# Optimization experiments

Hardware: AMD Instinct MI355X
Metric: run time of the kernel (lower is better)

The kernel has to match this reference:

```python
import jax, jax.numpy as jnp
import numpy as np

N = 50000
E = 800000
IN_C, C1, C2 = 256, 128, 64
BN_EPS = 1e-5


def setup_inputs() -> dict:
    key = jax.random.key(0)
    ks = jax.random.split(key, 12)
    x = jax.random.normal(ks[0], (N, IN_C), dtype=jnp.float32)
    edge_index = jax.random.randint(ks[1], (2, E), 0, N, dtype=jnp.int32)
    edge_weight = jax.random.uniform(ks[2], (E,), dtype=jnp.float32)
    W1 = jax.random.normal(ks[3], (IN_C, C1), dtype=jnp.float32) * 0.05
    b1 = jnp.zeros((C1,), dtype=jnp.float32)
    W2 = jax.random.normal(ks[4], (C1, C2), dtype=jnp.float32) * 0.05
    b2 = jnp.zeros((C2,), dtype=jnp.float32)
    g1 = jnp.ones((C1,), dtype=jnp.float32)
    be1 = jnp.zeros((C1,), dtype=jnp.float32)
    g2 = jnp.ones((C2,), dtype=jnp.float32)
    be2 = jnp.zeros((C2,), dtype=jnp.float32)
    Ws = jax.random.normal(ks[5], (IN_C, C2), dtype=jnp.float32) * 0.05
    bs = jnp.zeros((C2,), dtype=jnp.float32)
    return dict(x=x, edge_index=edge_index, edge_weight=edge_weight,
                W1=W1, b1=b1, W2=W2, b2=b2, g1=g1, be1=be1, g2=g2, be2=be2,
                Ws=Ws, bs=bs)


def _gcn_conv(h_in, row, col, ew, W, b):
    # PyG GCNConv: transform then symmetric-normalized aggregation with self-loops
    n = h_in.shape[0]
    h = h_in @ W  # [N, C]
    loop = jnp.arange(n, dtype=row.dtype)
    row_f = jnp.concatenate([row, loop])
    col_f = jnp.concatenate([col, loop])
    ew_f = jnp.concatenate([ew, jnp.ones((n,), dtype=ew.dtype)])
    deg = jax.ops.segment_sum(ew_f, col_f, num_segments=n)  # degree at targets
    dinv = jnp.where(deg > 0, jax.lax.rsqrt(deg), 0.0)
    norm = dinv[row_f] * ew_f * dinv[col_f]  # [E+N]
    out = jax.ops.segment_sum(h[row_f] * norm[:, None], col_f, num_segments=n)
    return out + b


def _batchnorm(x, gamma, beta):
    mu = jnp.mean(x, axis=0)
    var = jnp.mean(jnp.square(x - mu), axis=0)  # biased, as torch BN forward
    return (x - mu) * jax.lax.rsqrt(var + BN_EPS) * gamma + beta


def reference(x, edge_index, edge_weight, W1, b1, W2, b2, g1, be1, g2, be2, Ws, bs):
    row, col = edge_index[0], edge_index[1]
    skip = x @ Ws + bs
    x1 = _gcn_conv(x, row, col, edge_weight, W1, b1)
    x1 = jax.nn.gelu(_batchnorm(x1, g1, be1), approximate=False)
    # dropout is identity in deterministic/eval reference
    x2 = _gcn_conv(x1, row, col, edge_weight, W2, b2)
    x2 = _batchnorm(x2, g2, be2) + skip
    return x2
```

## Files before the change

### kernel.cpp

```cpp
#include <hip/hip_runtime.h>
#include <math.h>

constexpr int NN = 50000;
constexpr int EE = 800000;
constexpr int INC = 256, CC1 = 128, CC2 = 64;
constexpr int CAP = 56;

typedef short bf16x8 __attribute__((ext_vector_type(8)));
typedef float f32x4 __attribute__((ext_vector_type(4)));

__device__ __forceinline__ unsigned short f2bf(float f) {
    unsigned int u = __builtin_bit_cast(unsigned int, f);
    u = (u + 0x7FFFu + ((u >> 16) & 1u)) >> 16;
    return (unsigned short)u;
}
__device__ __forceinline__ float bf2f(unsigned short u) {
    return __builtin_bit_cast(float, (unsigned int)u << 16);
}
__device__ __forceinline__ float bflo(unsigned int w) {
    return __builtin_bit_cast(float, w << 16);
}
__device__ __forceinline__ float bfhi(unsigned int w) {
    return __builtin_bit_cast(float, w & 0xFFFF0000u);
}
__device__ __forceinline__ unsigned int packbf2(float lo, float hi) {
    return (unsigned int)f2bf(lo) | ((unsigned int)f2bf(hi) << 16);
}
__device__ __forceinline__ float dinv_of(unsigned long long pk) {
    return rsqrtf(1.0f + (float)(unsigned int)pk * (1.0f / 16777216.0f));
}

__global__ void zero_kernel(unsigned long long* __restrict__ packed,
                            float* __restrict__ stats) {
    int i = blockIdx.x * 256 + threadIdx.x;
    if (i < NN) packed[i] = 0ULL;
    if (i < 384) stats[i] = 0.0f;
}

__global__ void __launch_bounds__(256) gemm1_rank_kernel(
        const float* __restrict__ A, const float* __restrict__ B1, const float* __restrict__ B2,
        unsigned short* __restrict__ C1, unsigned short* __restrict__ C2,
        const int* __restrict__ row, const int* __restrict__ col, const float* __restrict__ ew,
        unsigned long long* __restrict__ packed, int2* __restrict__ pairs, int gemm_blocks) {
    constexpr int K = INC, N1 = CC1, N2 = CC2, NT = N1 + N2;
    constexpr int KC = K / 8, PITCH = K + 8;
    __shared__ unsigned short Blds[64 * PITCH];

    if ((int)blockIdx.x >= gemm_blocks) {
        int e = (blockIdx.x - gemm_blocks) * 256 + threadIdx.x;
        if (e < EE) {
            int c = col[e], r = row[e];
            float w = ew[e];
            unsigned int fx = __float2uint_rn(w * 16777216.0f);
            unsigned long long old =
                atomicAdd(&packed[c], (1ULL << 32) | (unsigned long long)fx);
            unsigned int rk = (unsigned int)(old >> 32);
            if (rk < CAP)
                pairs[(long long)c * CAP + rk] = make_int2(r, __float_as_int(w));
        }
        return;
    }

    const int tid = threadIdx.x;
    const int wave = tid >> 6, lane = tid & 63;
    const int quad = lane >> 4, nIdx = lane & 15;
    const int row0 = blockIdx.x * 64 + wave * 16;
    const int arow = row0 + nIdx;
    const int arow_c = (arow < NN) ? arow : (NN - 1);

    bf16x8 afrag[K / 32];
    {
        const float* ap = A + (long long)arow_c * K + quad * 8;
#pragma unroll
        for (int s = 0; s < K / 32; s++) {
            float4 lo = *(const float4*)(ap + s * 32);
            float4 hi = *(const float4*)(ap + s * 32 + 4);
            bf16x8 f;
            f[0] = (short)f2bf(lo.x); f[1] = (short)f2bf(lo.y);
            f[2] = (short)f2bf(lo.z); f[3] = (short)f2bf(lo.w);
            f[4] = (short)f2bf(hi.x); f[5] = (short)f2bf(hi.y);
            f[6] = (short)f2bf(hi.z); f[7] = (short)f2bf(hi.w);
            afrag[s] = f;
        }
    }

    for (int g0 = 0; g0 < NT; g0 += 64) {
        if (g0) __syncthreads();
        {
            int n = tid & 63;
            int gcol = g0 + n;
            const float* Bp = B1; int Nw = N1; int bcol = gcol;
            if (gcol >= N1) { Bp = B2; Nw = N2; bcol = gcol - N1; }
            for (int kc = tid >> 6; kc < KC; kc += 4) {
                int k0 = kc * 8;
                bf16x8 v;
#pragma unroll
                for (int j = 0; j < 8; j++)
                    v[j] = (short)f2bf(Bp[(long long)(k0 + j) * Nw + bcol]);
                *(bf16x8*)(&Blds[n * PITCH + k0]) = v;
            }
        }
        __syncthreads();
#pragma unroll
        for (int t4 = 0; t4 < 4; t4++) {
            const unsigned short* bp = &Blds[(t4 * 16 + nIdx) * PITCH + quad * 8];
            f32x4 acc = {0.0f, 0.0f, 0.0f, 0.0f};
#pragma unroll
            for (int s = 0; s < K / 32; s++) {
                bf16x8 bf = *(const bf16x8*)(bp + s * 32);
                acc = __builtin_amdgcn_mfma_f32_16x16x32_bf16(afrag[s], bf, acc, 0, 0, 0);
            }
            int ocol = g0 + t4 * 16 + nIdx;
#pragma unroll
            for (int r = 0; r < 4; r++) {
                int orow = row0 + quad * 4 + r;
                if (orow < NN) {
                    if (ocol < N1)
                        C1[(long long)orow * N1 + ocol] = f2bf(acc[r]);
                    else
                        C2[(long long)orow * N2 + (ocol - N1)] = f2bf(acc[r]);
                }
            }
        }
    }
}

__global__ void __launch_bounds__(256) gather1_kernel(
        const unsigned short* __restrict__ h, const unsigned long long* __restrict__ packed,
        const float* __restrict__ b1, const int2* __restrict__ pairs,
        unsigned short* __restrict__ aggb, float* __restrict__ stats) {
    const int tid = threadIdx.x;
    const int gi = blockIdx.x * 256 + tid;
    const int node = gi >> 4;
    const int part = tid & 15;
    const int c8 = part * 8;

    unsigned long long pk = packed[node];
    int m = (int)(pk >> 32); if (m > CAP) m = CAP;
    float dc = dinv_of(pk);
    float d2 = dc * dc;

    uint4 hv = *(const uint4*)(h + (long long)node * CC1 + c8);
    float a0 = bflo(hv.x) * d2 + b1[c8 + 0];
    float a1 = bfhi(hv.x) * d2 + b1[c8 + 1];
    float a2 = bflo(hv.y) * d2 + b1[c8 + 2];
    float a3 = bfhi(hv.y) * d2 + b1[c8 + 3];
    float a4 = bflo(hv.z) * d2 + b1[c8 + 4];
    float a5 = bfhi(hv.z) * d2 + b1[c8 + 5];
    float a6 = bflo(hv.w) * d2 + b1[c8 + 6];
    float a7 = bfhi(hv.w) * d2 + b1[c8 + 7];

    const int2* pp = pairs + (long long)node * CAP;
    int j = 0;
    for (; j + 8 <= m; j += 8) {
        int2 p[8];
#pragma unroll
        for (int i = 0; i < 8; i++) p[i] = pp[j + i];
        unsigned long long pkr[8];
#pragma unroll
        for (int i = 0; i < 8; i++) pkr[i] = packed[p[i].x];
        uint4 v[8];
#pragma unroll
        for (int i = 0; i < 8; i++)
            v[i] = *(const uint4*)(h + (long long)p[i].x * CC1 + c8);
#pragma unroll
        for (int i = 0; i < 8; i++) {
            float w = dinv_of(pkr[i]) * __int_as_float(p[i].y) * dc;
            a0 += bflo(v[i].x) * w; a1 += bfhi(v[i].x) * w;
            a2 += bflo(v[i].y) * w; a3 += bfhi(v[i].y) * w;
            a4 += bflo(v[i].z) * w; a5 += bfhi(v[i].z) * w;
            a6 += bflo(v[i].w) * w; a7 += bfhi(v[i].w) * w;
        }
    }
    for (; j < m; j++) {
        int2 p = pp[j];
        float w = dinv_of(packed[p.x]) * __int_as_float(p.y) * dc;
        uint4 v = *(const uint4*)(h + (long long)p.x * CC1 + c8);
        a0 += bflo(v.x) * w; a1 += bfhi(v.x) * w;
        a2 += bflo(v.y) * w; a3 += bfhi(v.y) * w;
        a4 += bflo(v.z) * w; a5 += bfhi(v.z) * w;
        a6 += bflo(v.w) * w; a7 += bfhi(v.w) * w;
    }
    uint4 o;
    o.x = packbf2(a0, a1); o.y = packbf2(a2, a3);
    o.z = packbf2(a4, a5); o.w = packbf2(a6, a7);
    *(uint4*)(aggb + (long long)node * CC1 + c8) = o;

    float s[8] = {a0, a1, a2, a3, a4, a5, a6, a7};
    float q[8] = {a0*a0, a1*a1, a2*a2, a3*a3, a4*a4, a5*a5, a6*a6, a7*a7};
#pragma unroll
    for (int k = 0; k < 8; k++) {
        s[k] += __shfl_xor(s[k], 16, 64); s[k] += __shfl_xor(s[k], 32, 64);
        q[k] += __shfl_xor(q[k], 16, 64); q[k] += __shfl_xor(q[k], 32, 64);
    }
    __shared__ float red[1024];
    const int wave = tid >> 6, lane = tid & 63;
    if (lane < 16) {
#pragma unroll
        for (int k = 0; k < 8; k++) {
            red[wave * 128 + lane * 8 + k] = s[k];
            red[512 + wave * 128 + lane * 8 + k] = q[k];
        }
    }
    __syncthreads();
    if (tid < CC1) {
        float as = 0.0f, aq = 0.0f;
#pragma unroll
        for (int w = 0; w < 4; w++) { as += red[w * 128 + tid]; aq += red[512 + w * 128 + tid]; }
        atomicAdd(&stats[tid], as);
        atomicAdd(&stats[128 + tid], aq);
    }
}

__global__ void __launch_bounds__(256) gemm2_kernel(
        const unsigned short* __restrict__ A, const float* __restrict__ B,
        unsigned short* __restrict__ C,
        const float* __restrict__ stats,
        const float* __restrict__ gamma, const float* __restrict__ beta) {
    constexpr int K = CC1, N = CC2;
    constexpr int KC = K / 8, PITCH = K + 8;
    __shared__ unsigned short Blds[N * PITCH];
    __shared__ float scL[K], shL[K];

    const int tid = threadIdx.x;
    if (tid < K) {
        float inv_n = 1.0f / (float)NN;
        float mu = stats[tid] * inv_n;
        float var = fmaxf(stats[128 + tid] * inv_n - mu * mu, 0.0f);
        float sc = gamma[tid] * rsqrtf(var + 1e-5f);
        scL[tid] = sc; shL[tid] = beta[tid] - mu * sc;
    }
    {
        int n = tid & 63;
        for (int kc = tid >> 6; kc < KC; kc += 4) {
            int k0 = kc * 8;
            bf16x8 v;
#pragma unroll
            for (int j = 0; j < 8; j++)
                v[j] = (short)f2bf(B[(long long)(k0 + j) * N + n]);
            *(bf16x8*)(&Blds[n * PITCH + k0]) = v;
        }
    }
    __syncthreads();

    const int wave = tid >> 6, lane = tid & 63;
    const int quad = lane >> 4, nIdx = lane & 15;
    const int row0 = blockIdx.x * 64 + wave * 16;
    const int arow = row0 + nIdx;
    const int arow_c = (arow < NN) ? arow : (NN - 1);

    bf16x8 afrag[K / 32];
    {
        const unsigned short* ap = A + (long long)arow_c * K + quad * 8;
#pragma unroll
        for (int s = 0; s < K / 32; s++) {
            bf16x8 raw = *(const bf16x8*)(ap + s * 32);
            int kb = s * 32 + quad * 8;
            bf16x8 f;
#pragma unroll
            for (int j = 0; j < 8; j++) {
                float u = bf2f((unsigned short)raw[j]) * scL[kb + j] + shL[kb + j];
                float v = u * 0.5f * (1.0f + erff(u * 0.70710678f));
                f[j] = (short)f2bf(v);
            }
            afrag[s] = f;
        }
    }
#pragma unroll
    for (int t4 = 0; t4 < N / 16; t4++) {
        const unsigned short* bp = &Blds[(t4 * 16 + nIdx) * PITCH + quad * 8];
        f32x4 acc = {0.0f, 0.0f, 0.0f, 0.0f};
#pragma unroll
        for (int s = 0; s < K / 32; s++) {
            bf16x8 bf = *(const bf16x8*)(bp + s * 32);
            acc = __builtin_amdgcn_mfma_f32_16x16x32_bf16(afrag[s], bf, acc, 0, 0, 0);
        }
        int ocol = t4 * 16 + nIdx;
#pragma unroll
        for (int r = 0; r < 4; r++) {
            int orow = row0 + quad * 4 + r;
            if (orow < NN)
                C[(long long)orow * N + ocol] = f2bf(acc[r]);
        }
    }
}

__global__ void __launch_bounds__(256) gather2_kernel(
        const unsigned short* __restrict__ h, const unsigned long long* __restrict__ packed,
        const float* __restrict__ b2, const int2* __restrict__ pairs,
        unsigned short* __restrict__ aggb, float* __restrict__ stats) {
    const int tid = threadIdx.x;
    const int gi = blockIdx.x * 256 + tid;
    const int node = gi >> 3;
    const int part = tid & 7;
    const int c8 = part * 8;

    float a0 = 0, a1 = 0, a2 = 0, a3 = 0, a4 = 0, a5 = 0, a6 = 0, a7 = 0;
    if (node < NN) {
        unsigned long long pk = packed[node];
        int m = (int)(pk >> 32); if (m > CAP) m = CAP;
        float dc = dinv_of(pk);
        float d2 = dc * dc;
        uint4 hv = *(const uint4*)(h + (long long)node * CC2 + c8);
        a0 = bflo(hv.x) * d2 + b2[c8 + 0];
        a1 = bfhi(hv.x) * d2 + b2[c8 + 1];
        a2 = bflo(hv.y) * d2 + b2[c8 + 2];
        a3 = bfhi(hv.y) * d2 + b2[c8 + 3];
        a4 = bflo(hv.z) * d2 + b2[c8 + 4];
        a5 = bfhi(hv.z) * d2 + b2[c8 + 5];
        a6 = bflo(hv.w) * d2 + b2[c8 + 6];
        a7 = bfhi(hv.w) * d2 + b2[c8 + 7];
        const int2* pp = pairs + (long long)node * CAP;
        int j = 0;
        for (; j + 8 <= m; j += 8) {
            int2 p[8];
#pragma unroll
            for (int i = 0; i < 8; i++) p[i] = pp[j + i];
            unsigned long long pkr[8];
#pragma unroll
            for (int i = 0; i < 8; i++) pkr[i] = packed[p[i].x];
            uint4 v[8];
#pragma unroll
            for (int i = 0; i < 8; i++)
                v[i] = *(const uint4*)(h + (long long)p[i].x * CC2 + c8);
#pragma unroll
            for (int i = 0; i < 8; i++) {
                float w = dinv_of(pkr[i]) * __int_as_float(p[i].y) * dc;
                a0 += bflo(v[i].x) * w; a1 += bfhi(v[i].x) * w;
                a2 += bflo(v[i].y) * w; a3 += bfhi(v[i].y) * w;
                a4 += bflo(v[i].z) * w; a5 += bfhi(v[i].z) * w;
                a6 += bflo(v[i].w) * w; a7 += bfhi(v[i].w) * w;
            }
        }
        for (; j < m; j++) {
            int2 p = pp[j];
            float w = dinv_of(packed[p.x]) * __int_as_float(p.y) * dc;
            uint4 v = *(const uint4*)(h + (long long)p.x * CC2 + c8);
            a0 += bflo(v.x) * w; a1 += bfhi(v.x) * w;
            a2 += bflo(v.y) * w; a3 += bfhi(v.y) * w;
            a4 += bflo(v.z) * w; a5 += bfhi(v.z) * w;
            a6 += bflo(v.w) * w; a7 += bfhi(v.w) * w;
        }
        uint4 o;
        o.x = packbf2(a0, a1); o.y = packbf2(a2, a3);
        o.z = packbf2(a4, a5); o.w = packbf2(a6, a7);
        *(uint4*)(aggb + (long long)node * CC2 + c8) = o;
    }

    float s[8] = {a0, a1, a2, a3, a4, a5, a6, a7};
    float q[8] = {a0*a0, a1*a1, a2*a2, a3*a3, a4*a4, a5*a5, a6*a6, a7*a7};
#pragma unroll
    for (int k = 0; k < 8; k++) {
        s[k] += __shfl_xor(s[k], 8, 64);
        s[k] += __shfl_xor(s[k], 16, 64);
        s[k] += __shfl_xor(s[k], 32, 64);
        q[k] += __shfl_xor(q[k], 8, 64);
        q[k] += __shfl_xor(q[k], 16, 64);
        q[k] += __shfl_xor(q[k], 32, 64);
    }
    __shared__ float red[512];
    const int wave = tid >> 6, lane = tid & 63;
    if (lane < 8) {
#pragma unroll
        for (int k = 0; k < 8; k++) {
            red[wave * 64 + lane * 8 + k] = s[k];
            red[256 + wave * 64 + lane * 8 + k] = q[k];
        }
    }
    __syncthreads();
    if (tid < CC2) {
        float as = 0.0f, aq = 0.0f;
#pragma unroll
        for (int w = 0; w < 4; w++) { as += red[w * 64 + tid]; aq += red[256 + w * 64 + tid]; }
        atomicAdd(&stats[256 + tid], as);
        atomicAdd(&stats[320 + tid], aq);
    }
}

__global__ void final_kernel(const unsigned short* __restrict__ agg2b,
                             const unsigned short* __restrict__ skipb,
                             const float* __restrict__ stats,
                             const float* __restrict__ gamma, const float* __restrict__ beta,
                             const float* __restrict__ bs, float* __restrict__ out) {
    __shared__ float sc[CC2], sh[CC2];
    if (threadIdx.x < CC2) {
        float inv_n = 1.0f / (float)NN;
        float mu = stats[256 + threadIdx.x] * inv_n;
        float var = fmaxf(stats[320 + threadIdx.x] * inv_n - mu * mu, 0.0f);
        float s = gamma[threadIdx.x] * rsqrtf(var + 1e-5f);
        sc[threadIdx.x] = s;
        sh[threadIdx.x] = beta[threadIdx.x] - mu * s + bs[threadIdx.x];
    }
    __syncthreads();
    int i2 = blockIdx.x * 256 + threadIdx.x;
    unsigned int av = ((const unsigned int*)agg2b)[i2];
    unsigned int sv = ((const unsigned int*)skipb)[i2];
    int c2 = (i2 & 31) * 2;
    float2 o;
    o.x = bflo(av) * sc[c2] + sh[c2] + bflo(sv);
    o.y = bfhi(av) * sc[c2 + 1] + sh[c2 + 1] + bfhi(sv);
    *(float2*)(out + 2 * (long long)i2) = o;
}


extern "C" void kernel_launch(void* const* d_in, const int* in_sizes, int n_in,
                              void* d_out, int out_size, void* d_ws, size_t ws_size,
                              hipStream_t stream) {
    const float* x   = (const float*)d_in[0];
    const int*   ei  = (const int*)d_in[1];
    const float* ew  = (const float*)d_in[2];
    const float* W1  = (const float*)d_in[3];
    const float* b1  = (const float*)d_in[4];
    const float* W2  = (const float*)d_in[5];
    const float* b2  = (const float*)d_in[6];
    const float* g1  = (const float*)d_in[7];
    const float* be1 = (const float*)d_in[8];
    const float* g2  = (const float*)d_in[9];
    const float* be2 = (const float*)d_in[10];
    const float* Ws  = (const float*)d_in[11];
    const float* bs  = (const float*)d_in[12];
    float* out = (float*)d_out;

    const int* row = ei;
    const int* col = ei + EE;

    char* wp = (char*)d_ws;
    float* stats = (float*)wp;
    unsigned long long* packed = (unsigned long long*)(wp + 4096);
    char* q = wp + 4096 + (size_t)NN * 8;
    int2* pairs = (int2*)q;                 q += (size_t)NN * CAP * 8;
    unsigned short* h1b = (unsigned short*)q;  q += (size_t)NN * CC1 * 2;
    unsigned short* h2b = h1b;
    unsigned short* agg1b = (unsigned short*)q; q += (size_t)NN * CC1 * 2;
    unsigned short* agg2b = agg1b;
    unsigned short* skipb = (unsigned short*)q; q += (size_t)NN * CC2 * 2;

    const int nb_G = (NN + 63) / 64;
    const int nb_E = (EE + 255) / 256;

    zero_kernel<<<(NN + 255) / 256, 256, 0, stream>>>(packed, stats);

    gemm1_rank_kernel<<<nb_G + nb_E, 256, 0, stream>>>(
        x, W1, Ws, h1b, skipb, row, col, ew, packed, pairs, nb_G);

    gather1_kernel<<<NN * 16 / 256, 256, 0, stream>>>(h1b, packed, b1, pairs, agg1b, stats);

    gemm2_kernel<<<nb_G, 256, 0, stream>>>(agg1b, W2, h2b, stats, g1, be1);

    gather2_kernel<<<(NN * 8 + 255) / 256, 256, 0, stream>>>(h2b, packed, b2, pairs, agg2b, stats);

    final_kernel<<<NN * (CC2 / 2) / 256, 256, 0, stream>>>(
        agg2b, skipb, stats, g2, be2, bs, out);

    (void)in_sizes; (void)n_in; (void)out_size; (void)ws_size;
}
```

Before: 322.5 us.

## Prenormalize edge weights by source dinv and use persistent grids for gathers

Adds a pass that folds each neighbour's inverse-sqrt degree into its stored edge weight once, so both gather kernels skip the per-edge random load of the neighbour's packed degree word. The gather kernels become grid-stride persistent loops (1024 and 784 blocks) that accumulate BN statistics in registers across nodes, which cuts the number of shared-memory reductions and global stat atomics. The cost is an extra kernel that reads and rewrites the whole pairs buffer (NN*CAP entries) plus fewer blocks in flight for latency hiding.

```diff
diff --git a/kernel.cpp b/kernel.cpp
--- a/kernel.cpp
+++ b/kernel.cpp
@@ -125,69 +125,91 @@
     }
 }
 
+__global__ void normalize_kernel(const unsigned long long* __restrict__ packed,
+                                 int2* __restrict__ pairs) {
+    int idx = blockIdx.x * 256 + threadIdx.x;
+    if (idx >= NN * CAP) return;
+    int node = idx / CAP;
+    int slot = idx - node * CAP;
+    int m = (int)(packed[node] >> 32); if (m > CAP) m = CAP;
+    if (slot < m) {
+        int2 p = pairs[idx];
+        float w = __int_as_float(p.y) * dinv_of(packed[p.x]);
+        pairs[idx].y = __float_as_int(w);
+    }
+}
+
+constexpr int CH1 = NN * 16 / 256;
 __global__ void __launch_bounds__(256) gather1_kernel(
         const unsigned short* __restrict__ h, const unsigned long long* __restrict__ packed,
         const float* __restrict__ b1, const int2* __restrict__ pairs,
         unsigned short* __restrict__ aggb, float* __restrict__ stats) {
     const int tid = threadIdx.x;
-    const int gi = blockIdx.x * 256 + tid;
-    const int node = gi >> 4;
     const int part = tid & 15;
     const int c8 = part * 8;
-
-    unsigned long long pk = packed[node];
-    int m = (int)(pk >> 32); if (m > CAP) m = CAP;
-    float dc = dinv_of(pk);
-    float d2 = dc * dc;
-
-    uint4 hv = *(const uint4*)(h + (long long)node * CC1 + c8);
-    float a0 = bflo(hv.x) * d2 + b1[c8 + 0];
-    float a1 = bfhi(hv.x) * d2 + b1[c8 + 1];
-    float a2 = bflo(hv.y) * d2 + b1[c8 + 2];
-    float a3 = bfhi(hv.y) * d2 + b1[c8 + 3];
-    float a4 = bflo(hv.z) * d2 + b1[c8 + 4];
-    float a5 = bfhi(hv.z) * d2 + b1[c8 + 5];
-    float a6 = bflo(hv.w) * d2 + b1[c8 + 6];
-    float a7 = bfhi(hv.w) * d2 + b1[c8 + 7];
-
-    const int2* pp = pairs + (long long)node * CAP;
-    int j = 0;
-    for (; j + 8 <= m; j += 8) {
-        int2 p[8];
-#pragma unroll
-        for (int i = 0; i < 8; i++) p[i] = pp[j + i];
-        unsigned long long pkr[8];
-#pragma unroll
-        for (int i = 0; i < 8; i++) pkr[i] = packed[p[i].x];
-        uint4 v[8];
-#pragma unroll
-        for (int i = 0; i < 8; i++)
-            v[i] = *(const uint4*)(h + (long long)p[i].x * CC1 + c8);
-#pragma unroll
-        for (int i = 0; i < 8; i++) {
-            float w = dinv_of(pkr[i]) * __int_as_float(p[i].y) * dc;
-            a0 += bflo(v[i].x) * w; a1 += bfhi(v[i].x) * w;
-            a2 += bflo(v[i].y) * w; a3 += bfhi(v[i].y) * w;
-            a4 += bflo(v[i].z) * w; a5 += bfhi(v[i].z) * w;
-            a6 += bflo(v[i].w) * w; a7 += bfhi(v[i].w) * w;
-        }
-    }
-    for (; j < m; j++) {
-        int2 p = pp[j];
-        float w = dinv_of(packed[p.x]) * __int_as_float(p.y) * dc;
-        uint4 v = *(const uint4*)(h + (long long)p.x * CC1 + c8);
-        a0 += bflo(v.x) * w; a1 += bfhi(v.x) * w;
-        a2 += bflo(v.y) * w; a3 += bfhi(v.y) * w;
-        a4 += bflo(v.z) * w; a5 += bfhi(v.z) * w;
-        a6 += bflo(v.w) * w; a7 += bfhi(v.w) * w;
-    }
-    uint4 o;
-    o.x = packbf2(a0, a1); o.y = packbf2(a2, a3);
-    o.z = packbf2(a4, a5); o.w = packbf2(a6, a7);
-    *(uint4*)(aggb + (long long)node * CC1 + c8) = o;
-
-    float s[8] = {a0, a1, a2, a3, a4, a5, a6, a7};
-    float q[8] = {a0*a0, a1*a1, a2*a2, a3*a3, a4*a4, a5*a5, a6*a6, a7*a7};
+    const int G = gridDim.x;
+
+    float s[8] = {0,0,0,0,0,0,0,0}, q[8] = {0,0,0,0,0,0,0,0};
+    float bb[8];
+#pragma unroll
+    for (int k = 0; k < 8; k++) bb[k] = b1[c8 + k];
+
+    for (int c = blockIdx.x; c < CH1; c += G) {
+        const int node = (c * 256 + tid) >> 4;
+        unsigned long long pk = packed[node];
+        int m = (int)(pk >> 32); if (m > CAP) m = CAP;
+        float dc = dinv_of(pk);
+        float d2 = dc * dc;
+
+        uint4 hv = *(const uint4*)(h + (long long)node * CC1 + c8);
+        float a0 = bflo(hv.x) * d2 + bb[0];
+        float a1 = bfhi(hv.x) * d2 + bb[1];
+        float a2 = bflo(hv.y) * d2 + bb[2];
+        float a3 = bfhi(hv.y) * d2 + bb[3];
+        float a4 = bflo(hv.z) * d2 + bb[4];
+        float a5 = bfhi(hv.z) * d2 + bb[5];
+        float a6 = bflo(hv.w) * d2 + bb[6];
+        float a7 = bfhi(hv.w) * d2 + bb[7];
+
+        const int2* pp = pairs + (long long)node * CAP;
+        int j = 0;
+        for (; j + 8 <= m; j += 8) {
+            int2 p[8];
+#pragma unroll
+            for (int i = 0; i < 8; i++) p[i] = pp[j + i];
+            uint4 v[8];
+#pragma unroll
+            for (int i = 0; i < 8; i++)
+                v[i] = *(const uint4*)(h + (long long)p[i].x * CC1 + c8);
+#pragma unroll
+            for (int i = 0; i < 8; i++) {
+                float w = __int_as_float(p[i].y) * dc;
+                a0 += bflo(v[i].x) * w; a1 += bfhi(v[i].x) * w;
+                a2 += bflo(v[i].y) * w; a3 += bfhi(v[i].y) * w;
+                a4 += bflo(v[i].z) * w; a5 += bfhi(v[i].z) * w;
+                a6 += bflo(v[i].w) * w; a7 += bfhi(v[i].w) * w;
+            }
+        }
+        for (; j < m; j++) {
+            int2 p = pp[j];
+            float w = __int_as_float(p.y) * dc;
+            uint4 v = *(const uint4*)(h + (long long)p.x * CC1 + c8);
+            a0 += bflo(v.x) * w; a1 += bfhi(v.x) * w;
+            a2 += bflo(v.y) * w; a3 += bfhi(v.y) * w;
+            a4 += bflo(v.z) * w; a5 += bfhi(v.z) * w;
+            a6 += bflo(v.w) * w; a7 += bfhi(v.w) * w;
+        }
+        uint4 o;
+        o.x = packbf2(a0, a1); o.y = packbf2(a2, a3);
+        o.z = packbf2(a4, a5); o.w = packbf2(a6, a7);
+        *(uint4*)(aggb + (long long)node * CC1 + c8) = o;
+
+        s[0] += a0; q[0] += a0 * a0; s[1] += a1; q[1] += a1 * a1;
+        s[2] += a2; q[2] += a2 * a2; s[3] += a3; q[3] += a3 * a3;
+        s[4] += a4; q[4] += a4 * a4; s[5] += a5; q[5] += a5 * a5;
+        s[6] += a6; q[6] += a6 * a6; s[7] += a7; q[7] += a7 * a7;
+    }
+
 #pragma unroll
     for (int k = 0; k < 8; k++) {
         s[k] += __shfl_xor(s[k], 16, 64); s[k] += __shfl_xor(s[k], 32, 64);
@@ -285,47 +307,50 @@
     }
 }
 
+constexpr int CH2 = (NN * 8 + 255) / 256;
 __global__ void __launch_bounds__(256) gather2_kernel(
         const unsigned short* __restrict__ h, const unsigned long long* __restrict__ packed,
         const float* __restrict__ b2, const int2* __restrict__ pairs,
         unsigned short* __restrict__ aggb, float* __restrict__ stats) {
     const int tid = threadIdx.x;
-    const int gi = blockIdx.x * 256 + tid;
-    const int node = gi >> 3;
     const int part = tid & 7;
     const int c8 = part * 8;
-
-    float a0 = 0, a1 = 0, a2 = 0, a3 = 0, a4 = 0, a5 = 0, a6 = 0, a7 = 0;
-    if (node < NN) {
+    const int G = gridDim.x;
+
+    float s[8] = {0,0,0,0,0,0,0,0}, q[8] = {0,0,0,0,0,0,0,0};
+    float bb[8];
+#pragma unroll
+    for (int k = 0; k < 8; k++) bb[k] = b2[c8 + k];
+
+    for (int c = blockIdx.x; c < CH2; c += G) {
+        const int node = (c * 256 + tid) >> 3;
+        if (node >= NN) continue;
         unsigned long long pk = packed[node];
         int m = (int)(pk >> 32); if (m > CAP) m = CAP;
         float dc = dinv_of(pk);
         float d2 = dc * dc;
         uint4 hv = *(const uint4*)(h + (long long)node * CC2 + c8);
-        a0 = bflo(hv.x) * d2 + b2[c8 + 0];
-        a1 = bfhi(hv.x) * d2 + b2[c8 + 1];
-        a2 = bflo(hv.y) * d2 + b2[c8 + 2];
-        a3 = bfhi(hv.y) * d2 + b2[c8 + 3];
-        a4 = bflo(hv.z) * d2 + b2[c8 + 4];
-        a5 = bfhi(hv.z) * d2 + b2[c8 + 5];
-        a6 = bflo(hv.w) * d2 + b2[c8 + 6];
-        a7 = bfhi(hv.w) * d2 + b2[c8 + 7];
+        float a0 = bflo(hv.x) * d2 + bb[0];
+        float a1 = bfhi(hv.x) * d2 + bb[1];
+        float a2 = bflo(hv.y) * d2 + bb[2];
+        float a3 = bfhi(hv.y) * d2 + bb[3];
+        float a4 = bflo(hv.z) * d2 + bb[4];
+        float a5 = bfhi(hv.z) * d2 + bb[5];
+        float a6 = bflo(hv.w) * d2 + bb[6];
+        float a7 = bfhi(hv.w) * d2 + bb[7];
         const int2* pp = pairs + (long long)node * CAP;
         int j = 0;
         for (; j + 8 <= m; j += 8) {
             int2 p[8];
 #pragma unroll
             for (int i = 0; i < 8; i++) p[i] = pp[j + i];
-            unsigned long long pkr[8];
-#pragma unroll
-            for (int i = 0; i < 8; i++) pkr[i] = packed[p[i].x];
             uint4 v[8];
 #pragma unroll
             for (int i = 0; i < 8; i++)
                 v[i] = *(const uint4*)(h + (long long)p[i].x * CC2 + c8);
 #pragma unroll
             for (int i = 0; i < 8; i++) {
-                float w = dinv_of(pkr[i]) * __int_as_float(p[i].y) * dc;
+                float w = __int_as_float(p[i].y) * dc;
                 a0 += bflo(v[i].x) * w; a1 += bfhi(v[i].x) * w;
                 a2 += bflo(v[i].y) * w; a3 += bfhi(v[i].y) * w;
                 a4 += bflo(v[i].z) * w; a5 += bfhi(v[i].z) * w;
@@ -334,7 +359,7 @@
         }
         for (; j < m; j++) {
             int2 p = pp[j];
-            float w = dinv_of(packed[p.x]) * __int_as_float(p.y) * dc;
+            float w = __int_as_float(p.y) * dc;
             uint4 v = *(const uint4*)(h + (long long)p.x * CC2 + c8);
             a0 += bflo(v.x) * w; a1 += bfhi(v.x) * w;
             a2 += bflo(v.y) * w; a3 += bfhi(v.y) * w;
@@ -345,10 +370,12 @@
         o.x = packbf2(a0, a1); o.y = packbf2(a2, a3);
         o.z = packbf2(a4, a5); o.w = packbf2(a6, a7);
         *(uint4*)(aggb + (long long)node * CC2 + c8) = o;
-    }
-
-    float s[8] = {a0, a1, a2, a3, a4, a5, a6, a7};
-    float q[8] = {a0*a0, a1*a1, a2*a2, a3*a3, a4*a4, a5*a5, a6*a6, a7*a7};
+        s[0] += a0; q[0] += a0 * a0; s[1] += a1; q[1] += a1 * a1;
+        s[2] += a2; q[2] += a2 * a2; s[3] += a3; q[3] += a3 * a3;
+        s[4] += a4; q[4] += a4 * a4; s[5] += a5; q[5] += a5 * a5;
+        s[6] += a6; q[6] += a6 * a6; s[7] += a7; q[7] += a7 * a7;
+    }
+
 #pragma unroll
     for (int k = 0; k < 8; k++) {
         s[k] += __shfl_xor(s[k], 8, 64);
@@ -443,11 +470,13 @@
     gemm1_rank_kernel<<<nb_G + nb_E, 256, 0, stream>>>(
         x, W1, Ws, h1b, skipb, row, col, ew, packed, pairs, nb_G);
 
-    gather1_kernel<<<NN * 16 / 256, 256, 0, stream>>>(h1b, packed, b1, pairs, agg1b, stats);
+    normalize_kernel<<<(NN * CAP + 255) / 256, 256, 0, stream>>>(packed, pairs);
+
+    gather1_kernel<<<1024, 256, 0, stream>>>(h1b, packed, b1, pairs, agg1b, stats);
 
     gemm2_kernel<<<nb_G, 256, 0, stream>>>(agg1b, W2, h2b, stats, g1, be1);
 
-    gather2_kernel<<<(NN * 8 + 255) / 256, 256, 0, stream>>>(h2b, packed, b2, pairs, agg2b, stats);
+    gather2_kernel<<<784, 256, 0, stream>>>(h2b, packed, b2, pairs, agg2b, stats);
 
     final_kernel<<<NN * (CC2 / 2) / 256, 256, 0, stream>>>(
         agg2b, skipb, stats, g2, be2, bs, out);
```

Result: faster. 295.5 us (-8.4%).
